# Kernel tuning notes

Measured on AMD Instinct MI355X. Metric: run time of the kernel, lower is better.

## Reference

```python
import jax, jax.numpy as jnp
import numpy as np

H, P, G, NS, K = 8, 64, 64, 64, 3          # heads, dim_head, slice_num, d_state, d_conv
D_INNER = H * P                            # 512
CONV_DIM = D_INNER + 2 * NS                # 640
D_IN_PROJ = 2 * D_INNER + 2 * NS + 2 * H   # 1168


def setup_inputs() -> dict:
    key = jax.random.key(0)
    ks = jax.random.split(key, 10)
    dim, Bsz, N = 256, 4, 8192
    s = 0.02
    return {
        "x": jax.random.normal(ks[0], (Bsz, N, dim), jnp.float32),
        "W_fx": jax.random.normal(ks[1], (D_INNER, dim), jnp.float32) * s,
        "b_fx": jnp.zeros((D_INNER,), jnp.float32),
        "W_x": jax.random.normal(ks[2], (D_INNER, dim), jnp.float32) * s,
        "b_x": jnp.zeros((D_INNER,), jnp.float32),
        "W_slice": jax.random.normal(ks[3], (G, P), jnp.float32) * s,
        "b_slice": jnp.zeros((G,), jnp.float32),
        "temperature": jnp.full((1, H, 1, 1), 0.5, jnp.float32),
        "hy_in_w": jax.random.normal(ks[4], (D_IN_PROJ, D_INNER), jnp.float32) * s,
        "hy_conv_w": jax.random.normal(ks[5], (CONV_DIM, K), jnp.float32) * s,
        "hy_conv_b": jnp.zeros((CONV_DIM,), jnp.float32),
        "hy_dt_bias": jnp.log(jnp.expm1(jnp.full((H,), 0.01, jnp.float32))),
        "hy_A_log": jnp.log(jnp.linspace(1.0, 16.0, H)).astype(jnp.float32),
        "hy_D": jnp.ones((H,), jnp.float32),
        "hy_fcD_w": jax.random.normal(ks[6], (H, D_INNER), jnp.float32) * s,
        "hy_norm_w": jnp.ones((D_INNER,), jnp.float32),
        "hy_out_w": jax.random.normal(ks[7], (D_INNER, D_INNER), jnp.float32) * s,
        "out_w": jax.random.normal(ks[8], (dim, D_INNER), jnp.float32) * s,
        "out_b": jnp.zeros((dim,), jnp.float32),
    }


def _hydra(u, in_w, conv_w, conv_b, dt_bias, A_log, Dp, fcD_w, norm_w, out_w):
    # Bidirectional Mamba2-style selective scan (Hydra, non mem-eff path).
    Bt, L, _ = u.shape
    zxbcdt = u @ in_w.T                                   # (B, L, 1168)
    z = zxbcdt[..., :D_INNER]
    xBC = zxbcdt[..., D_INNER:D_INNER + CONV_DIM]
    dt = zxbcdt[..., -2 * H:]
    # fwd dts for fwd copies, time-flipped bwd dts stacked along batch
    dt = jnp.concatenate([dt[..., :H], jnp.flip(dt[..., H:], axis=1)], axis=0)
    dt = jax.nn.softplus(dt + dt_bias)                    # (2B, L, H)
    # depthwise causal conv, kernel K, left pad K-1 then silu
    xp = jnp.pad(xBC, ((0, 0), (K - 1, 0), (0, 0)))
    xBC = sum(xp[:, k:k + L, :] * conv_w[:, k] for k in range(K)) + conv_b
    xBC = jax.nn.silu(xBC)
    x = xBC[..., :D_INNER]
    Bm = xBC[..., D_INNER:D_INNER + NS]
    Cm = xBC[..., D_INNER + NS:]
    x_og = x
    x2 = jnp.concatenate([x, jnp.flip(x, 1)], 0).reshape(2 * Bt, L, H, P)
    B2 = jnp.concatenate([Bm, jnp.flip(Bm, 1)], 0)        # (2B, L, NS)
    C2 = jnp.concatenate([Cm, jnp.flip(Cm, 1)], 0)
    dA = jnp.exp(dt * (-jnp.exp(A_log)))                  # (2B, L, H)
    dBx = jnp.einsum('blh,bln,blhp->blhpn', dt, B2, x2)   # (2B, L, H, P, NS)

    def step(h, inp):
        dA_t, dBx_t, C_t = inp
        h = h * dA_t[:, :, None, None] + dBx_t
        return h, jnp.einsum('bhpn,bn->bhp', h, C_t)

    h0 = jnp.zeros((2 * Bt, H, P, NS), u.dtype)
    _, ys = jax.lax.scan(step, h0, (dA.transpose(1, 0, 2), dBx.transpose(1, 0, 2, 3, 4), C2.transpose(1, 0, 2)))
    y = ys.transpose(1, 0, 2, 3).reshape(2 * Bt, L, D_INNER)
    y_fw, y_bw = y[:Bt], jnp.flip(y[Bt:], 1)
    # quasiseparable: strictly-lower (shift fwd) + strictly-upper (shift bwd) + diagonal
    y = jnp.pad(y_fw[:, :-1], ((0, 0), (1, 0), (0, 0))) + jnp.pad(y_bw[:, 1:], ((0, 0), (0, 1), (0, 0)))
    y = y + x_og * jnp.repeat(x_og @ fcD_w.T + Dp, P, axis=-1)
    # gated RMSNorm (gate before norm), then out projection
    yg = y * jax.nn.silu(z)
    yg = yg * jax.lax.rsqrt(jnp.mean(jnp.square(yg), -1, keepdims=True) + 1e-5) * norm_w
    return yg @ out_w.T


def reference(x, W_fx, b_fx, W_x, b_x, W_slice, b_slice, temperature,
              hy_in_w, hy_conv_w, hy_conv_b, hy_dt_bias, hy_A_log, hy_D,
              hy_fcD_w, hy_norm_w, hy_out_w, out_w, out_b):
    B, N, _ = x.shape
    fx = (x @ W_fx.T + b_fx).reshape(B, N, H, P).transpose(0, 2, 1, 3)   # (B,H,N,P)
    xm = (x @ W_x.T + b_x).reshape(B, N, H, P).transpose(0, 2, 1, 3)
    temp = jnp.maximum(temperature, 1e-6)
    sw = jax.nn.softmax((xm @ W_slice.T + b_slice) / temp, axis=-1)      # (B,H,N,G)
    snorm = sw.sum(2)                                                     # (B,H,G)
    st = jnp.einsum('bhnc,bhng->bhgc', fx, sw) / (snorm + 1e-5)[..., None]
    st = st.transpose(0, 2, 1, 3).reshape(B, G, D_INNER)                  # (B,G,512)
    ot = _hydra(st, hy_in_w, hy_conv_w, hy_conv_b, hy_dt_bias, hy_A_log, hy_D,
                hy_fcD_w, hy_norm_w, hy_out_w)
    ot = ot.reshape(B, G, H, P).transpose(0, 2, 1, 3)                     # (B,H,G,P)
    out = jnp.einsum('bhgc,bhng->bhnc', ot, sw).transpose(0, 2, 1, 3).reshape(B, N, D_INNER)
    return out @ out_w.T + out_b
```

## Files before the change

kernel.cpp:

```cpp
#include <hip/hip_runtime.h>
#include <hip/hip_bf16.h>
#include <cstdint>
#include <cstddef>

#define Hh 8
#define DIN 512
#define CONVD 640
#define DPROJ 1168
#define NTOK 8192
#define DIM 256

typedef __attribute__((ext_vector_type(8))) short short8;
typedef __attribute__((ext_vector_type(4))) float f32x4;

static __device__ __forceinline__ float sigmoidf_(float x) { return 1.f / (1.f + expf(-x)); }
static __device__ __forceinline__ unsigned short f2b(float f) {
  __hip_bfloat16 h = __float2bfloat16(f);
  return *(unsigned short*)&h;
}
static __device__ __forceinline__ float b2f(unsigned short u) {
  union { unsigned int i; float f; } cv; cv.i = ((unsigned int)u) << 16; return cv.f;
}
static __device__ __forceinline__ void gll16(const void* g, void* l) {
  __builtin_amdgcn_global_load_lds((const __attribute__((address_space(1))) void*)g,
                                   (__attribute__((address_space(3))) void*)l, 16, 0, 0);
}

__global__ __launch_bounds__(256) void k_cvt(
    const float* __restrict__ wfx, const float* __restrict__ wx, const float* __restrict__ outw,
    const float* __restrict__ inw, const float* __restrict__ how,
    const float* __restrict__ bfx, const float* __restrict__ bx,
    const float* __restrict__ x,
    unsigned short* __restrict__ wcat, unsigned short* __restrict__ outwb,
    unsigned short* __restrict__ inwb, unsigned short* __restrict__ howb,
    float* __restrict__ bcat, unsigned short* __restrict__ xb) {
  const int blk = blockIdx.x;
  if (blk < 4096) {
    const int e = (blk * 256 + threadIdx.x) * 8;
    float4 v0 = *(const float4*)(x + e);
    float4 v1 = *(const float4*)(x + e + 4);
    short8 o;
    o[0] = (short)f2b(v0.x); o[1] = (short)f2b(v0.y);
    o[2] = (short)f2b(v0.z); o[3] = (short)f2b(v0.w);
    o[4] = (short)f2b(v1.x); o[5] = (short)f2b(v1.y);
    o[6] = (short)f2b(v1.z); o[7] = (short)f2b(v1.w);
    *(short8*)(xb + e) = o;
    return;
  }
  const int e = ((blk - 4096) * 256 + threadIdx.x) * 4;
  if (e >= 1253376) {
    const int i = e - 1253376;
    float4 v;
    if (i < 512) v = *(const float4*)(bfx + i);
    else         v = *(const float4*)(bx + (i - 512));
    *(float4*)(bcat + i) = v;
    return;
  }
  const float* src; unsigned short* dst; int i;
  if (e < 131072)        { i = e;           src = wfx;  dst = wcat; }
  else if (e < 262144)   { i = e - 131072;  src = wx;   dst = wcat + 131072; }
  else if (e < 393216)   { i = e - 262144;  src = outw; dst = outwb; }
  else if (e < 991232)   { i = e - 393216;  src = inw;  dst = inwb; }
  else                   { i = e - 991232;  src = how;  dst = howb; }
  float4 v = *(const float4*)(src + i);
  ushort4 o;
  o.x = f2b(v.x); o.y = f2b(v.y); o.z = f2b(v.z); o.w = f2b(v.w);
  *(ushort4*)(dst + i) = o;
}

__global__ __launch_bounds__(256) void k_front(
    const unsigned short* __restrict__ xb, const unsigned short* __restrict__ wcat,
    const float* __restrict__ bcat, const float* __restrict__ Wslice,
    const float* __restrict__ bslice, const float* __restrict__ temperature,
    unsigned short* __restrict__ swb, float* __restrict__ st_part,
    float* __restrict__ sn_part) {
  __shared__ unsigned short lds[34816];
  const int tid = threadIdx.x;
  const int m0 = blockIdx.x * 128;
  const int h = blockIdx.y;
  const int w = tid >> 6, lane = tid & 63;
  const int l15 = lane & 15, kq = lane >> 4;
  const int wm = (w & 1) * 64, wn = (w >> 1) * 64;
  const int bbase = (wn == 0) ? h * 64 : 512 + h * 64;
  float bs[4];
#pragma unroll
  for (int j = 0; j < 4; ++j) bs[j] = bcat[bbase + j * 16 + l15];
  f32x4 acc[4][4];
#pragma unroll
  for (int i = 0; i < 4; ++i)
#pragma unroll
    for (int j = 0; j < 4; ++j) acc[i][j] = (f32x4){0.f, 0.f, 0.f, 0.f};

  auto stage = [&](int buf, int kt) {
    unsigned short* As = lds + buf * 8192;
    unsigned short* Bs = lds + 16384 + buf * 8192;
#pragma unroll
    for (int i = 0; i < 4; ++i) {
      const int c = tid + 256 * i;
      const int m = c >> 3, kb = c & 7;
      const int kbs = (kb ^ (m & 7)) * 8;
      gll16(&xb[(size_t)(m0 + m) * 256 + kt + kbs], &As[c * 8]);
      const int wr = (m < 64) ? (h * 64 + m) : (448 + h * 64 + m);
      gll16(&wcat[(size_t)wr * 256 + kt + kbs], &Bs[c * 8]);
    }
  };

  stage(0, 0);
  __syncthreads();
  int buf = 0;
  for (int t = 0; t < 4; ++t) {
    if (t < 3) stage(buf ^ 1, (t + 1) * 64);
    const unsigned short* As = lds + buf * 8192;
    const unsigned short* Bs = lds + 16384 + buf * 8192;
#pragma unroll
    for (int kw = 0; kw < 2; ++kw) {
      short8 af[4], bfr[4];
#pragma unroll
      for (int i = 0; i < 4; ++i) {
        const int rm = wm + i * 16 + l15;
        af[i]  = *(const short8*)&As[rm * 64 + ((kw * 32 + kq * 8) ^ ((rm & 7) << 3))];
        const int rn = wn + i * 16 + l15;
        bfr[i] = *(const short8*)&Bs[rn * 64 + ((kw * 32 + kq * 8) ^ ((rn & 7) << 3))];
      }
#pragma unroll
      for (int i = 0; i < 4; ++i)
#pragma unroll
        for (int j = 0; j < 4; ++j)
          acc[i][j] = __builtin_amdgcn_mfma_f32_16x16x32_bf16(af[i], bfr[j], acc[i][j], 0, 0, 0);
    }
    __syncthreads();
    buf ^= 1;
  }
  unsigned short* Cs = lds;
#pragma unroll
  for (int i = 0; i < 4; ++i)
#pragma unroll
    for (int j = 0; j < 4; ++j)
#pragma unroll
      for (int r = 0; r < 4; ++r) {
        const int m = wm + i * 16 + kq * 4 + r;
        const int n = wn + j * 16 + l15;
        Cs[m * 136 + n] = f2b(acc[i][j][r] + bs[j]);
      }
  __syncthreads();

  short8 sbfr[2][4];
#pragma unroll
  for (int kt = 0; kt < 2; ++kt)
#pragma unroll
    for (int j = 0; j < 4; ++j) {
      const float* wp = Wslice + (j * 16 + l15) * 64 + kt * 32 + kq * 8;
      short8 t;
#pragma unroll
      for (int u = 0; u < 8; ++u) t[u] = (short)f2b(wp[u]);
      sbfr[kt][j] = t;
    }
  float sbs[4];
#pragma unroll
  for (int j = 0; j < 4; ++j) sbs[j] = bslice[j * 16 + l15];
  f32x4 sacc[2][4];
#pragma unroll
  for (int i = 0; i < 2; ++i)
#pragma unroll
    for (int j = 0; j < 4; ++j) sacc[i][j] = (f32x4){0.f, 0.f, 0.f, 0.f};
#pragma unroll
  for (int kt = 0; kt < 2; ++kt) {
    short8 af[2];
#pragma unroll
    for (int i = 0; i < 2; ++i)
      af[i] = *(const short8*)&Cs[(w * 32 + i * 16 + l15) * 136 + 64 + kt * 32 + kq * 8];
#pragma unroll
    for (int i = 0; i < 2; ++i)
#pragma unroll
      for (int j = 0; j < 4; ++j)
        sacc[i][j] = __builtin_amdgcn_mfma_f32_16x16x32_bf16(af[i], sbfr[kt][j], sacc[i][j], 0, 0, 0);
  }
  __syncthreads();

  unsigned short* swT = lds + 17408;
  unsigned short* fxT = lds + 26112;
  const float invt = 1.f / fmaxf(temperature[h], 1e-6f);
#pragma unroll
  for (int i = 0; i < 2; ++i)
#pragma unroll
    for (int r = 0; r < 4; ++r) {
      float v[4];
      float m = -1e30f;
#pragma unroll
      for (int j = 0; j < 4; ++j) { v[j] = (sacc[i][j][r] + sbs[j]) * invt; m = fmaxf(m, v[j]); }
#pragma unroll
      for (int off = 8; off; off >>= 1) m = fmaxf(m, __shfl_xor(m, off));
      float s = 0.f;
#pragma unroll
      for (int j = 0; j < 4; ++j) { v[j] = expf(v[j] - m); s += v[j]; }
#pragma unroll
      for (int off = 8; off; off >>= 1) s += __shfl_xor(s, off);
      const float inv = 1.f / s;
      const int row = w * 32 + i * 16 + kq * 4 + r;
#pragma unroll
      for (int j = 0; j < 4; ++j) {
        const unsigned short us = f2b(v[j] * inv);
        Cs[row * 136 + 64 + j * 16 + l15] = us;
        swT[(j * 16 + l15) * 136 + row] = us;
      }
    }
#pragma unroll
  for (int i = 0; i < 4; ++i) {
    const int c = tid + 256 * i;
    const int n = c >> 3, pc = c & 7;
    const short8 t = *(const short8*)&Cs[n * 136 + pc * 8];
#pragma unroll
    for (int u = 0; u < 8; ++u) fxT[(pc * 8 + u) * 136 + n] = (unsigned short)t[u];
  }
  __syncthreads();

  short8 ones;
#pragma unroll
  for (int u = 0; u < 8; ++u) ones[u] = (short)0x3F80;
  f32x4 st_acc[4];
  f32x4 accO = (f32x4){0.f, 0.f, 0.f, 0.f};
#pragma unroll
  for (int j = 0; j < 4; ++j) st_acc[j] = (f32x4){0.f, 0.f, 0.f, 0.f};
#pragma unroll
  for (int kt = 0; kt < 4; ++kt) {
    const short8 af = *(const short8*)&swT[(w * 16 + l15) * 136 + kt * 32 + kq * 8];
#pragma unroll
    for (int j = 0; j < 4; ++j) {
      const short8 bf = *(const short8*)&fxT[(j * 16 + l15) * 136 + kt * 32 + kq * 8];
      st_acc[j] = __builtin_amdgcn_mfma_f32_16x16x32_bf16(af, bf, st_acc[j], 0, 0, 0);
    }
    accO = __builtin_amdgcn_mfma_f32_16x16x32_bf16(af, ones, accO, 0, 0, 0);
  }

  const int bidx = m0 >> 13, nb = m0 & (NTOK - 1);
  const int bh = bidx * 8 + h;
#pragma unroll
  for (int it = 0; it < 4; ++it) {
    const int c = tid + 256 * it;
    const int n = c >> 3, seg = c & 7;
    *(short8*)&swb[((size_t)bh * NTOK + nb + n) * 64 + seg * 8] =
        *(const short8*)&Cs[n * 136 + 64 + seg * 8];
  }

  const int chunk = blockIdx.x & 15;
  float* stp = st_part + ((size_t)(chunk * 32 + bh)) * 4096;
  const int g = w * 16 + kq * 4;
#pragma unroll
  for (int j = 0; j < 4; ++j)
#pragma unroll
    for (int r = 0; r < 4; ++r)
      atomicAdd(&stp[(g + r) * 64 + j * 16 + l15], st_acc[j][r]);
  if (l15 == 0) {
    float* snp = sn_part + ((size_t)(chunk * 32 + bh)) * 64;
#pragma unroll
    for (int r = 0; r < 4; ++r)
      atomicAdd(&snp[g + r], accO[r]);
  }
}

__global__ __launch_bounds__(256) void k_stnorm(
    const float* __restrict__ st_part, const float* __restrict__ sn_part,
    unsigned short* __restrict__ st2b) {
  const int idx = blockIdx.x * 256 + threadIdx.x;
  const int p = idx & 63, g = (idx >> 6) & 63, h = (idx >> 12) & 7, b = idx >> 15;
  const int bh = idx >> 12;
  const int gp = idx & 4095;
  float s = 0.f, sn = 0.f;
#pragma unroll
  for (int bx = 0; bx < 16; ++bx) {
    s  += st_part[((size_t)bx * 32 + bh) * 4096 + gp];
    sn += sn_part[((size_t)bx * 32 + bh) * 64 + g];
  }
  const float v = s / (sn + 1e-5f);
  st2b[(size_t)(b * 64 + g) * DIN + h * 64 + p] = f2b(v);
}

__global__ __launch_bounds__(256) void k_inproj(
    const unsigned short* __restrict__ st2b, const unsigned short* __restrict__ inwb,
    float* __restrict__ zx) {
  const int tid = threadIdx.x;
  const int m0 = blockIdx.x * 64;
  const int n0 = blockIdx.y * 64;
  const int w = tid >> 6, lane = tid & 63;
  const int l15 = lane & 15, kq = lane >> 4;
  f32x4 acc[4];
#pragma unroll
  for (int j = 0; j < 4; ++j) acc[j] = (f32x4){0.f, 0.f, 0.f, 0.f};
  const int arow = m0 + w * 16 + l15;
#pragma unroll
  for (int kc = 0; kc < 16; ++kc) {
    const short8 af = *(const short8*)&st2b[(size_t)arow * DIN + kc * 32 + kq * 8];
#pragma unroll
    for (int j = 0; j < 4; ++j) {
      int brow = n0 + j * 16 + l15;
      if (brow >= DPROJ) brow = 0;
      const short8 bfr = *(const short8*)&inwb[(size_t)brow * DIN + kc * 32 + kq * 8];
      acc[j] = __builtin_amdgcn_mfma_f32_16x16x32_bf16(af, bfr, acc[j], 0, 0, 0);
    }
  }
#pragma unroll
  for (int j = 0; j < 4; ++j)
#pragma unroll
    for (int r = 0; r < 4; ++r) {
      const int m = m0 + w * 16 + kq * 4 + r;
      const int c = n0 + j * 16 + l15;
      if (c < DPROJ) zx[(size_t)m * DPROJ + c] = acc[j][r];
    }
}

__global__ __launch_bounds__(256) void k_prep(
    const float* __restrict__ zx, const float* __restrict__ convw, const float* __restrict__ convb,
    const float* __restrict__ dtbias, const float* __restrict__ Alog,
    float* __restrict__ xbc, float* __restrict__ dt2, float* __restrict__ ldA2) {
  const int idx = blockIdx.x * 256 + threadIdx.x;
  const int NCONV = 4 * 64 * CONVD;
  if (idx < NCONV) {
    const int c = idx % CONVD;
    const int l = (idx / CONVD) & 63;
    const int b = idx / (CONVD * 64);
    float acc = convb[c];
#pragma unroll
    for (int k = 0; k < 3; ++k) {
      const int ls = l - 2 + k;
      if (ls >= 0) acc += zx[(size_t)(b * 64 + ls) * DPROJ + DIN + c] * convw[c * 3 + k];
    }
    xbc[idx] = acc * sigmoidf_(acc);
  } else if (idx < NCONV + 8 * 64 * 8) {
    const int j = idx - NCONV;
    const int h = j & 7, l = (j >> 3) & 63, bb = j >> 9;
    float raw;
    if (bb < 4) raw = zx[(size_t)(bb * 64 + l) * DPROJ + 1152 + h];
    else        raw = zx[(size_t)((bb - 4) * 64 + (63 - l)) * DPROJ + 1160 + h];
    const float d = raw + dtbias[h];
    const float sp = (d > 20.f) ? d : log1pf(expf(d));
    dt2[j] = sp;
    ldA2[j] = sp * -expf(Alog[h]);
  }
}

__global__ __launch_bounds__(256) void k_ssm(
    const float* __restrict__ xbc, const float* __restrict__ dt2, const float* __restrict__ ldA2,
    float* __restrict__ ys) {
  __shared__ unsigned short s_C[64][72];
  __shared__ unsigned short s_Bm[64][72];
  __shared__ unsigned short s_X[64][72];
  __shared__ unsigned short s_G[64][72];
  __shared__ float s_L[64];
  __shared__ float s_dt[64];
  const int blk = blockIdx.x;
  const int h = blk & 7, bb = blk >> 3;
  const int b = (bb < 4) ? bb : bb - 4;
  const bool rev = bb >= 4;
  const int tid = threadIdx.x;
  const int w = tid >> 6, lane = tid & 63;
  const int l15 = lane & 15, kq = lane >> 4;
  {
    const int l = tid >> 2, part = tid & 3;
    const int t = rev ? 63 - l : l;
    const float* src = xbc + (size_t)(b * 64 + l) * CONVD + DIN + part * 32;
#pragma unroll
    for (int u = 0; u < 32; u += 4) {
      float4 v = *(const float4*)(src + u);
      const int c = part * 32 + u;
      unsigned short* dst = (c < 64) ? &s_Bm[t][c] : &s_C[t][c - 64];
      dst[0] = f2b(v.x); dst[1] = f2b(v.y); dst[2] = f2b(v.z); dst[3] = f2b(v.w);
    }
    const float* xs = xbc + (size_t)(b * 64 + l) * CONVD + h * 64 + part * 16;
#pragma unroll
    for (int u = 0; u < 16; u += 4) {
      float4 v = *(const float4*)(xs + u);
      const int p = part * 16 + u;
      s_X[p + 0][t] = f2b(v.x); s_X[p + 1][t] = f2b(v.y);
      s_X[p + 2][t] = f2b(v.z); s_X[p + 3][t] = f2b(v.w);
    }
  }
  if (w == 0) {
    const float dtv = dt2[(bb * 64 + lane) * 8 + h];
    float ld = ldA2[(bb * 64 + lane) * 8 + h];
#pragma unroll
    for (int off = 1; off < 64; off <<= 1) {
      const float o = __shfl_up(ld, off);
      if (lane >= off) ld += o;
    }
    s_L[lane] = ld;
    s_dt[lane] = dtv;
  }
  __syncthreads();
  f32x4 accS[4];
#pragma unroll
  for (int i = 0; i < 4; ++i) accS[i] = (f32x4){0.f, 0.f, 0.f, 0.f};
#pragma unroll
  for (int kw = 0; kw < 2; ++kw) {
    const short8 bfr = *(const short8*)&s_Bm[w * 16 + l15][kw * 32 + kq * 8];
#pragma unroll
    for (int i = 0; i < 4; ++i) {
      const short8 af = *(const short8*)&s_C[i * 16 + l15][kw * 32 + kq * 8];
      accS[i] = __builtin_amdgcn_mfma_f32_16x16x32_bf16(af, bfr, accS[i], 0, 0, 0);
    }
  }
  const int s_idx = w * 16 + l15;
  const float Ls = s_L[s_idx];
  const float dts = s_dt[s_idx];
#pragma unroll
  for (int i = 0; i < 4; ++i)
#pragma unroll
    for (int r = 0; r < 4; ++r) {
      const int t = i * 16 + kq * 4 + r;
      const float g = (s_idx <= t) ? accS[i][r] * expf(s_L[t] - Ls) * dts : 0.f;
      s_G[t][s_idx] = f2b(g);
    }
  __syncthreads();
  f32x4 accY[4];
#pragma unroll
  for (int i = 0; i < 4; ++i) accY[i] = (f32x4){0.f, 0.f, 0.f, 0.f};
#pragma unroll
  for (int kw = 0; kw < 2; ++kw) {
    const short8 bfr = *(const short8*)&s_X[w * 16 + l15][kw * 32 + kq * 8];
#pragma unroll
    for (int i = 0; i < 4; ++i) {
      const short8 af = *(const short8*)&s_G[i * 16 + l15][kw * 32 + kq * 8];
      accY[i] = __builtin_amdgcn_mfma_f32_16x16x32_bf16(af, bfr, accY[i], 0, 0, 0);
    }
  }
#pragma unroll
  for (int i = 0; i < 4; ++i)
#pragma unroll
    for (int r = 0; r < 4; ++r) {
      const int t = i * 16 + kq * 4 + r;
      ys[(((size_t)(bb * 64 + t) * 8 + h) << 6) + w * 16 + l15] = accY[i][r];
    }
}

__global__ __launch_bounds__(256) void k_gate(
    const float* __restrict__ ys, const float* __restrict__ xbc, const float* __restrict__ zx,
    const float* __restrict__ fcdw, const float* __restrict__ Dp,
    const float* __restrict__ normw, unsigned short* __restrict__ ygb) {
  __shared__ float red[256][9];
  __shared__ float s_xfc[8];
  const int bl = blockIdx.x;
  const int b = bl >> 6, l = bl & 63;
  const int tid = threadIdx.x;
  const float xog0 = xbc[(size_t)bl * CONVD + tid];
  const float xog1 = xbc[(size_t)bl * CONVD + 256 + tid];
#pragma unroll
  for (int h = 0; h < 8; ++h)
    red[tid][h] = xog0 * fcdw[h * DIN + tid] + xog1 * fcdw[h * DIN + 256 + tid];
  __syncthreads();
  for (int s = 128; s > 0; s >>= 1) {
    if (tid < s) {
#pragma unroll
      for (int h = 0; h < 8; ++h) red[tid][h] += red[tid + s][h];
    }
    __syncthreads();
  }
  if (tid < 8) s_xfc[tid] = red[0][tid] + Dp[tid];
  __syncthreads();
  float ygv[2];
  float sumsq = 0.f;
#pragma unroll
  for (int ci = 0; ci < 2; ++ci) {
    const int c = tid + ci * 256;
    const int h = c >> 6, p = c & 63;
    float yv = 0.f;
    if (l >= 1)  yv += ys[(((size_t)(b * 64 + (l - 1)) * 8 + h) << 6) + p];
    if (l <= 62) yv += ys[(((size_t)((4 + b) * 64 + (62 - l)) * 8 + h) << 6) + p];
    const float xog = (ci == 0) ? xog0 : xog1;
    yv += xog * s_xfc[h];
    const float z = zx[(size_t)bl * DPROJ + c];
    const float g = yv * (z * sigmoidf_(z));
    ygv[ci] = g;
    sumsq += g * g;
  }
  red[tid][0] = sumsq;
  __syncthreads();
  for (int s = 128; s > 0; s >>= 1) {
    if (tid < s) red[tid][0] += red[tid + s][0];
    __syncthreads();
  }
  const float scale = 1.f / sqrtf(red[0][0] / 512.f + 1e-5f);
#pragma unroll
  for (int ci = 0; ci < 2; ++ci) {
    const int c = tid + ci * 256;
    ygb[(size_t)bl * DIN + c] = f2b(ygv[ci] * scale * normw[c]);
  }
}

__global__ __launch_bounds__(256) void k_oproj(
    const unsigned short* __restrict__ ygb, const unsigned short* __restrict__ howb,
    unsigned short* __restrict__ otT) {
  __shared__ unsigned short Cs[64][72];
  const int tid = threadIdx.x;
  const int b = blockIdx.x;
  const int h = blockIdx.y;
  const int m0 = b * 64, n0 = h * 64;
  const int w = tid >> 6, lane = tid & 63;
  const int l15 = lane & 15, kq = lane >> 4;
  f32x4 acc[4];
#pragma unroll
  for (int j = 0; j < 4; ++j) acc[j] = (f32x4){0.f, 0.f, 0.f, 0.f};
  const int arow = m0 + w * 16 + l15;
#pragma unroll
  for (int kc = 0; kc < 16; ++kc) {
    const short8 af = *(const short8*)&ygb[(size_t)arow * DIN + kc * 32 + kq * 8];
#pragma unroll
    for (int j = 0; j < 4; ++j) {
      const int brow = n0 + j * 16 + l15;
      const short8 bfr = *(const short8*)&howb[(size_t)brow * DIN + kc * 32 + kq * 8];
      acc[j] = __builtin_amdgcn_mfma_f32_16x16x32_bf16(af, bfr, acc[j], 0, 0, 0);
    }
  }
#pragma unroll
  for (int j = 0; j < 4; ++j)
#pragma unroll
    for (int r = 0; r < 4; ++r) {
      const int g = w * 16 + kq * 4 + r;
      const int p = j * 16 + l15;
      Cs[p][g] = f2b(acc[j][r]);
    }
  __syncthreads();
#pragma unroll
  for (int it = 0; it < 2; ++it) {
    const int c = tid + 256 * it;
    const int p = c >> 3, seg = c & 7;
    *(short8*)&otT[(((size_t)(b * 8 + h) * 64 + p) << 6) + seg * 8] = *(const short8*)&Cs[p][seg * 8];
  }
}

__global__ __launch_bounds__(256) void k_mixfinal(
    const unsigned short* __restrict__ swb, const unsigned short* __restrict__ otT,
    const unsigned short* __restrict__ outwb, const float* __restrict__ outb,
    float* __restrict__ out) {
  __shared__ unsigned short lm[33280];
  const int blk = blockIdx.x;
  const int b = blk >> 7;
  const int t0 = (blk & 127) * 64;
  const int tid = threadIdx.x;
  const int w = tid >> 6, lane = tid & 63;
  const int l15 = lane & 15, kq = lane >> 4;
#pragma unroll
  for (int hh = 0; hh < 2; ++hh) {
    const int h = w * 2 + hh;
    const int bh = b * 8 + h;
    f32x4 acc[4][4];
#pragma unroll
    for (int i = 0; i < 4; ++i)
#pragma unroll
      for (int j = 0; j < 4; ++j) acc[i][j] = (f32x4){0.f, 0.f, 0.f, 0.f};
#pragma unroll
    for (int kt = 0; kt < 2; ++kt) {
      short8 af[4], bfr[4];
#pragma unroll
      for (int i = 0; i < 4; ++i) {
        af[i]  = *(const short8*)&swb[((size_t)bh * NTOK + t0 + i * 16 + l15) * 64 + kt * 32 + kq * 8];
        bfr[i] = *(const short8*)&otT[(((size_t)bh * 64 + i * 16 + l15) << 6) + kt * 32 + kq * 8];
      }
#pragma unroll
      for (int i = 0; i < 4; ++i)
#pragma unroll
        for (int j = 0; j < 4; ++j)
          acc[i][j] = __builtin_amdgcn_mfma_f32_16x16x32_bf16(af[i], bfr[j], acc[i][j], 0, 0, 0);
    }
#pragma unroll
    for (int i = 0; i < 4; ++i)
#pragma unroll
      for (int j = 0; j < 4; ++j)
#pragma unroll
        for (int r = 0; r < 4; ++r)
          lm[(i * 16 + kq * 4 + r) * 520 + h * 64 + j * 16 + l15] = f2b(acc[i][j][r]);
  }
  __syncthreads();
  float ob[4];
#pragma unroll
  for (int j = 0; j < 4; ++j) ob[j] = outb[w * 64 + j * 16 + l15];
  f32x4 facc[4][4];
#pragma unroll
  for (int i = 0; i < 4; ++i)
#pragma unroll
    for (int j = 0; j < 4; ++j) facc[i][j] = (f32x4){0.f, 0.f, 0.f, 0.f};
#pragma unroll
  for (int kt = 0; kt < 16; ++kt) {
    short8 af[4], bfr[4];
#pragma unroll
    for (int i = 0; i < 4; ++i) {
      af[i]  = *(const short8*)&lm[(i * 16 + l15) * 520 + kt * 32 + kq * 8];
      bfr[i] = *(const short8*)&outwb[(size_t)(w * 64 + i * 16 + l15) * 512 + kt * 32 + kq * 8];
    }
#pragma unroll
    for (int i = 0; i < 4; ++i)
#pragma unroll
      for (int j = 0; j < 4; ++j)
        facc[i][j] = __builtin_amdgcn_mfma_f32_16x16x32_bf16(af[i], bfr[j], facc[i][j], 0, 0, 0);
  }
  __syncthreads();
  float* lf = (float*)lm;
#pragma unroll
  for (int i = 0; i < 4; ++i)
#pragma unroll
    for (int j = 0; j < 4; ++j)
#pragma unroll
      for (int r = 0; r < 4; ++r)
        lf[(i * 16 + kq * 4 + r) * 260 + w * 64 + j * 16 + l15] = facc[i][j][r] + ob[j];
  __syncthreads();
#pragma unroll
  for (int it = 0; it < 16; ++it) {
    const int c = tid + 256 * it;
    const int row = c >> 6, seg = c & 63;
    *(float4*)&out[((size_t)(b * NTOK + t0 + row)) * 256 + seg * 4] =
        *(const float4*)&lf[row * 260 + seg * 4];
  }
}

extern "C" void kernel_launch(void* const* d_in, const int* in_sizes, int n_in,
                              void* d_out, int out_size, void* d_ws, size_t ws_size,
                              hipStream_t stream) {
  const float* x      = (const float*)d_in[0];
  const float* Wfx    = (const float*)d_in[1];
  const float* bfx    = (const float*)d_in[2];
  const float* Wx     = (const float*)d_in[3];
  const float* bx     = (const float*)d_in[4];
  const float* Wslice = (const float*)d_in[5];
  const float* bslice = (const float*)d_in[6];
  const float* temp   = (const float*)d_in[7];
  const float* inw    = (const float*)d_in[8];
  const float* convw  = (const float*)d_in[9];
  const float* convb  = (const float*)d_in[10];
  const float* dtbias = (const float*)d_in[11];
  const float* Alog   = (const float*)d_in[12];
  const float* Dp     = (const float*)d_in[13];
  const float* fcdw   = (const float*)d_in[14];
  const float* normw  = (const float*)d_in[15];
  const float* how    = (const float*)d_in[16];
  const float* outw   = (const float*)d_in[17];
  const float* outb   = (const float*)d_in[18];

  unsigned short* us = (unsigned short*)d_ws;
  unsigned short* swb    = us;
  unsigned short* wcatb  = swb + 16777216;
  unsigned short* outwbf = wcatb + 262144;
  unsigned short* otTb   = outwbf + 131072;
  unsigned short* inwb   = otTb + 131072;
  unsigned short* howb   = inwb + 598016;
  unsigned short* st2b   = howb + 262144;
  unsigned short* ygbb   = st2b + 131072;
  unsigned short* xbb    = ygbb + 131072;
  float* fbase = (float*)(xbb + 8388608);
  float* bcat    = fbase;
  float* st_part = bcat + 1024;
  float* sn_part = st_part + 2097152;
  float* zx      = sn_part + 32768;
  float* xbc     = zx + 299008;
  float* dt2     = xbc + 163840;
  float* ldA2    = dt2 + 4096;
  float* ysb     = ldA2 + 4096;

  hipMemsetAsync(st_part, 0, (2097152 + 32768) * sizeof(float), stream);

  k_cvt     <<<dim3(5321),    256, 0, stream>>>(Wfx, Wx, outw, inw, how, bfx, bx, x,
                                                wcatb, outwbf, inwb, howb, bcat, xbb);
  k_front   <<<dim3(256, 8),  256, 0, stream>>>(xbb, wcatb, bcat, Wslice, bslice, temp,
                                                swb, st_part, sn_part);
  k_stnorm  <<<dim3(512),     256, 0, stream>>>(st_part, sn_part, st2b);
  k_inproj  <<<dim3(4, 19),   256, 0, stream>>>(st2b, inwb, zx);
  k_prep    <<<dim3(656),     256, 0, stream>>>(zx, convw, convb, dtbias, Alog, xbc, dt2, ldA2);
  k_ssm     <<<dim3(64),      256, 0, stream>>>(xbc, dt2, ldA2, ysb);
  k_gate    <<<dim3(256),     256, 0, stream>>>(ysb, xbc, zx, fcdw, Dp, normw, ygbb);
  k_oproj   <<<dim3(4, 8),    256, 0, stream>>>(ygbb, howb, otTb);
  k_mixfinal<<<dim3(512),     256, 0, stream>>>(swb, otTb, outwbf, outb, (float*)d_out);
}
```

Before: 266.2 us.

## Fuse conv/dt prep into in-proj, restructure front LDS epilogue, shuffle reductions in gate

The conv and dt preparation kernel is folded into the in-projection GEMM epilogue, so each block's tile stays in LDS and the zx round trip plus one launch go away. The front kernel now writes fx directly in transposed form and keeps the xm tile in a separate smaller buffer. This removes the extra LDS transpose pass and reduces the LDS footprint. The gate kernel replaces its shared-memory tree reductions with wave shuffles, cutting the number of barriers.

```diff
diff --git a/kernel.cpp b/kernel.cpp
--- a/kernel.cpp
+++ b/kernel.cpp
@@ -74,7 +74,7 @@
     const float* __restrict__ bslice, const float* __restrict__ temperature,
     unsigned short* __restrict__ swb, float* __restrict__ st_part,
     float* __restrict__ sn_part) {
-  __shared__ unsigned short lds[34816];
+  __shared__ unsigned short lds[32768];
   const int tid = threadIdx.x;
   const int m0 = blockIdx.x * 128;
   const int h = blockIdx.y;
@@ -131,17 +131,30 @@
     __syncthreads();
     buf ^= 1;
   }
-  unsigned short* Cs = lds;
-#pragma unroll
-  for (int i = 0; i < 4; ++i)
-#pragma unroll
-    for (int j = 0; j < 4; ++j)
-#pragma unroll
-      for (int r = 0; r < 4; ++r) {
-        const int m = wm + i * 16 + kq * 4 + r;
-        const int n = wn + j * 16 + l15;
-        Cs[m * 136 + n] = f2b(acc[i][j][r] + bs[j]);
+  unsigned short* fxT = lds;
+  unsigned short* Xs  = lds + 8704;
+  unsigned short* swT = lds + 17920;
+  if (wn == 0) {
+#pragma unroll
+    for (int i = 0; i < 4; ++i)
+#pragma unroll
+      for (int j = 0; j < 4; ++j) {
+        short4 pk;
+        pk.x = (short)f2b(acc[i][j][0] + bs[j]);
+        pk.y = (short)f2b(acc[i][j][1] + bs[j]);
+        pk.z = (short)f2b(acc[i][j][2] + bs[j]);
+        pk.w = (short)f2b(acc[i][j][3] + bs[j]);
+        *(short4*)&fxT[(j * 16 + l15) * 136 + wm + i * 16 + kq * 4] = pk;
       }
+  } else {
+#pragma unroll
+    for (int i = 0; i < 4; ++i)
+#pragma unroll
+      for (int j = 0; j < 4; ++j)
+#pragma unroll
+        for (int r = 0; r < 4; ++r)
+          Xs[(wm + i * 16 + kq * 4 + r) * 72 + j * 16 + l15] = f2b(acc[i][j][r] + bs[j]);
+  }
   __syncthreads();
 
   short8 sbfr[2][4];
@@ -168,7 +181,7 @@
     short8 af[2];
 #pragma unroll
     for (int i = 0; i < 2; ++i)
-      af[i] = *(const short8*)&Cs[(w * 32 + i * 16 + l15) * 136 + 64 + kt * 32 + kq * 8];
+      af[i] = *(const short8*)&Xs[(w * 32 + i * 16 + l15) * 72 + kt * 32 + kq * 8];
 #pragma unroll
     for (int i = 0; i < 2; ++i)
 #pragma unroll
@@ -177,8 +190,6 @@
   }
   __syncthreads();
 
-  unsigned short* swT = lds + 17408;
-  unsigned short* fxT = lds + 26112;
   const float invt = 1.f / fmaxf(temperature[h], 1e-6f);
 #pragma unroll
   for (int i = 0; i < 2; ++i)
@@ -200,18 +211,10 @@
 #pragma unroll
       for (int j = 0; j < 4; ++j) {
         const unsigned short us = f2b(v[j] * inv);
-        Cs[row * 136 + 64 + j * 16 + l15] = us;
+        Xs[row * 72 + j * 16 + l15] = us;
         swT[(j * 16 + l15) * 136 + row] = us;
       }
     }
-#pragma unroll
-  for (int i = 0; i < 4; ++i) {
-    const int c = tid + 256 * i;
-    const int n = c >> 3, pc = c & 7;
-    const short8 t = *(const short8*)&Cs[n * 136 + pc * 8];
-#pragma unroll
-    for (int u = 0; u < 8; ++u) fxT[(pc * 8 + u) * 136 + n] = (unsigned short)t[u];
-  }
   __syncthreads();
 
   short8 ones;
@@ -239,7 +242,7 @@
     const int c = tid + 256 * it;
     const int n = c >> 3, seg = c & 7;
     *(short8*)&swb[((size_t)bh * NTOK + nb + n) * 64 + seg * 8] =
-        *(const short8*)&Cs[n * 136 + 64 + seg * 8];
+        *(const short8*)&Xs[n * 72 + seg * 8];
   }
 
   const int chunk = blockIdx.x & 15;
@@ -277,10 +280,16 @@
 
 __global__ __launch_bounds__(256) void k_inproj(
     const unsigned short* __restrict__ st2b, const unsigned short* __restrict__ inwb,
-    float* __restrict__ zx) {
+    const float* __restrict__ convw, const float* __restrict__ convb,
+    const float* __restrict__ dtbias, const float* __restrict__ Alog,
+    float* __restrict__ zx, float* __restrict__ xbc,
+    float* __restrict__ dt2, float* __restrict__ ldA2) {
+  __shared__ float zs[64][65];
   const int tid = threadIdx.x;
-  const int m0 = blockIdx.x * 64;
-  const int n0 = blockIdx.y * 64;
+  const int b = blockIdx.x;
+  const int m0 = b * 64;
+  const int y = blockIdx.y;
+  const int n0 = y * 64;
   const int w = tid >> 6, lane = tid & 63;
   const int l15 = lane & 15, kq = lane >> 4;
   f32x4 acc[4];
@@ -298,41 +307,54 @@
       acc[j] = __builtin_amdgcn_mfma_f32_16x16x32_bf16(af, bfr, acc[j], 0, 0, 0);
     }
   }
+  if (y < 8) {
+#pragma unroll
+    for (int j = 0; j < 4; ++j)
+#pragma unroll
+      for (int r = 0; r < 4; ++r) {
+        const int m = m0 + w * 16 + kq * 4 + r;
+        const int c = n0 + j * 16 + l15;
+        zx[(size_t)m * DPROJ + c] = acc[j][r];
+      }
+    return;
+  }
 #pragma unroll
   for (int j = 0; j < 4; ++j)
 #pragma unroll
-    for (int r = 0; r < 4; ++r) {
-      const int m = m0 + w * 16 + kq * 4 + r;
-      const int c = n0 + j * 16 + l15;
-      if (c < DPROJ) zx[(size_t)m * DPROJ + c] = acc[j][r];
-    }
-}
-
-__global__ __launch_bounds__(256) void k_prep(
-    const float* __restrict__ zx, const float* __restrict__ convw, const float* __restrict__ convb,
-    const float* __restrict__ dtbias, const float* __restrict__ Alog,
-    float* __restrict__ xbc, float* __restrict__ dt2, float* __restrict__ ldA2) {
-  const int idx = blockIdx.x * 256 + threadIdx.x;
-  const int NCONV = 4 * 64 * CONVD;
-  if (idx < NCONV) {
-    const int c = idx % CONVD;
-    const int l = (idx / CONVD) & 63;
-    const int b = idx / (CONVD * 64);
-    float acc = convb[c];
-#pragma unroll
-    for (int k = 0; k < 3; ++k) {
-      const int ls = l - 2 + k;
-      if (ls >= 0) acc += zx[(size_t)(b * 64 + ls) * DPROJ + DIN + c] * convw[c * 3 + k];
-    }
-    xbc[idx] = acc * sigmoidf_(acc);
-  } else if (idx < NCONV + 8 * 64 * 8) {
-    const int j = idx - NCONV;
-    const int h = j & 7, l = (j >> 3) & 63, bb = j >> 9;
-    float raw;
-    if (bb < 4) raw = zx[(size_t)(bb * 64 + l) * DPROJ + 1152 + h];
-    else        raw = zx[(size_t)((bb - 4) * 64 + (63 - l)) * DPROJ + 1160 + h];
+    for (int r = 0; r < 4; ++r)
+      zs[w * 16 + kq * 4 + r][j * 16 + l15] = acc[j][r];
+  __syncthreads();
+  if (y < 18) {
+    const int cc0 = (y - 8) * 64;
+    const int l = tid >> 2, q = tid & 3;
+#pragma unroll
+    for (int u = 0; u < 16; u += 4) {
+      float4 o;
+      float* op = &o.x;
+#pragma unroll
+      for (int v = 0; v < 4; ++v) {
+        const int lc = q * 16 + u + v;
+        const int cc = cc0 + lc;
+        float a = convb[cc];
+#pragma unroll
+        for (int k = 0; k < 3; ++k) {
+          const int ls = l - 2 + k;
+          if (ls >= 0) a += zs[ls][lc] * convw[cc * 3 + k];
+        }
+        op[v] = a * sigmoidf_(a);
+      }
+      *(float4*)&xbc[((size_t)(b * 64 + l)) * CONVD + cc0 + q * 16 + u] = o;
+    }
+    return;
+  }
+#pragma unroll
+  for (int u = 0; u < 4; ++u) {
+    const int e = tid + 256 * u;
+    const int h = e & 7, l = (e >> 3) & 63, dir = e >> 9;
+    const float raw = (dir == 0) ? zs[l][h] : zs[63 - l][8 + h];
     const float d = raw + dtbias[h];
     const float sp = (d > 20.f) ? d : log1pf(expf(d));
+    const int j = ((dir ? (4 + b) : b) * 64 + l) * 8 + h;
     dt2[j] = sp;
     ldA2[j] = sp * -expf(Alog[h]);
   }
@@ -435,25 +457,29 @@
     const float* __restrict__ ys, const float* __restrict__ xbc, const float* __restrict__ zx,
     const float* __restrict__ fcdw, const float* __restrict__ Dp,
     const float* __restrict__ normw, unsigned short* __restrict__ ygb) {
-  __shared__ float red[256][9];
+  __shared__ float xw[4][8];
+  __shared__ float xs[4];
   __shared__ float s_xfc[8];
   const int bl = blockIdx.x;
   const int b = bl >> 6, l = bl & 63;
   const int tid = threadIdx.x;
+  const int w = tid >> 6, lane = tid & 63;
   const float xog0 = xbc[(size_t)bl * CONVD + tid];
   const float xog1 = xbc[(size_t)bl * CONVD + 256 + tid];
+  float p8[8];
 #pragma unroll
   for (int h = 0; h < 8; ++h)
-    red[tid][h] = xog0 * fcdw[h * DIN + tid] + xog1 * fcdw[h * DIN + 256 + tid];
-  __syncthreads();
-  for (int s = 128; s > 0; s >>= 1) {
-    if (tid < s) {
-#pragma unroll
-      for (int h = 0; h < 8; ++h) red[tid][h] += red[tid + s][h];
-    }
-    __syncthreads();
-  }
-  if (tid < 8) s_xfc[tid] = red[0][tid] + Dp[tid];
+    p8[h] = xog0 * fcdw[h * DIN + tid] + xog1 * fcdw[h * DIN + 256 + tid];
+#pragma unroll
+  for (int off = 32; off; off >>= 1)
+#pragma unroll
+    for (int h = 0; h < 8; ++h) p8[h] += __shfl_xor(p8[h], off);
+  if (lane == 0) {
+#pragma unroll
+    for (int h = 0; h < 8; ++h) xw[w][h] = p8[h];
+  }
+  __syncthreads();
+  if (tid < 8) s_xfc[tid] = xw[0][tid] + xw[1][tid] + xw[2][tid] + xw[3][tid] + Dp[tid];
   __syncthreads();
   float ygv[2];
   float sumsq = 0.f;
@@ -471,13 +497,12 @@
     ygv[ci] = g;
     sumsq += g * g;
   }
-  red[tid][0] = sumsq;
-  __syncthreads();
-  for (int s = 128; s > 0; s >>= 1) {
-    if (tid < s) red[tid][0] += red[tid + s][0];
-    __syncthreads();
-  }
-  const float scale = 1.f / sqrtf(red[0][0] / 512.f + 1e-5f);
+#pragma unroll
+  for (int off = 32; off; off >>= 1) sumsq += __shfl_xor(sumsq, off);
+  if (lane == 0) xs[w] = sumsq;
+  __syncthreads();
+  const float tot = xs[0] + xs[1] + xs[2] + xs[3];
+  const float scale = 1.f / sqrtf(tot / 512.f + 1e-5f);
 #pragma unroll
   for (int ci = 0; ci < 2; ++ci) {
     const int c = tid + ci * 256;
@@ -660,8 +685,8 @@
   k_front   <<<dim3(256, 8),  256, 0, stream>>>(xbb, wcatb, bcat, Wslice, bslice, temp,
                                                 swb, st_part, sn_part);
   k_stnorm  <<<dim3(512),     256, 0, stream>>>(st_part, sn_part, st2b);
-  k_inproj  <<<dim3(4, 19),   256, 0, stream>>>(st2b, inwb, zx);
-  k_prep    <<<dim3(656),     256, 0, stream>>>(zx, convw, convb, dtbias, Alog, xbc, dt2, ldA2);
+  k_inproj  <<<dim3(4, 19),   256, 0, stream>>>(st2b, inwb, convw, convb, dtbias, Alog,
+                                                zx, xbc, dt2, ldA2);
   k_ssm     <<<dim3(64),      256, 0, stream>>>(xbc, dt2, ldA2, ysb);
   k_gate    <<<dim3(256),     256, 0, stream>>>(ysb, xbc, zx, fcdw, Dp, normw, ygbb);
   k_oproj   <<<dim3(4, 8),    256, 0, stream>>>(ygbb, howb, otTb);
```

Result: faster. 259.0 us (median of 2 runs) (-2.7%).
